# Kernel optimization log

Hardware: AMD Instinct MI355X
Metric: run time of the kernel (lower is better)

The kernel has to match this reference:

```python
import jax, jax.numpy as jnp
import numpy as np
import math

NH, NKV, D = 32, 8, 128  # heads, kv heads, head dim

def _alibi_slopes(n):
    cp2 = 2 ** math.floor(math.log2(n))
    base = 2.0 ** (-8.0 / cp2)
    slopes = base ** np.arange(1, cp2 + 1, dtype=np.float32)
    if cp2 != n:
        extra_base = 2.0 ** (-4.0 / cp2)
        extra = extra_base ** np.arange(1, 1 + 2 * (n - cp2), 2, dtype=np.float32)
        slopes = np.concatenate([slopes, extra])
    return slopes.astype(np.float32)

def setup_inputs() -> dict:
    key = jax.random.key(0)
    k1, k2, k3 = jax.random.split(key, 3)
    B, S, H = 4, 1024, 4096
    qkv_out = NH * D + 2 * NKV * D  # 6144
    return {
        "hidden_states": jax.random.normal(k1, (B, S, H), jnp.float32) * 0.02,
        "w_qkv": jax.random.normal(k2, (H, qkv_out), jnp.float32) * 0.02,
        "w_o": jax.random.normal(k3, (NH * D, H), jnp.float32) * 0.02,
    }

def reference(hidden_states, w_qkv, w_o):
    B, S, H = hidden_states.shape
    G = NH // NKV  # query groups per kv head
    scale = D ** -0.5

    qkv = hidden_states @ w_qkv  # [B,S,6144]
    q = qkv[..., : NH * D].reshape(B, S, NKV, G, D)
    k = qkv[..., NH * D : NH * D + NKV * D].reshape(B, S, NKV, D)
    v = qkv[..., NH * D + NKV * D :].reshape(B, S, NKV, D)

    scores = jnp.einsum("bqhgd,bkhd->bhgqk", q, k) * scale  # [B,NKV,G,S,S]

    slopes = jnp.asarray(_alibi_slopes(NH)).reshape(NKV, G)  # head order
    pos = jnp.arange(S)
    rel = pos[:, None] - pos[None, :]  # i - j
    sqrt_dist = jnp.sqrt(jnp.maximum(rel, 0).astype(jnp.float32))
    bias = -slopes[:, :, None, None] * sqrt_dist  # ALiBi-sqrt bias
    bias = jnp.where(rel[None, None] >= 0, bias, -jnp.inf)  # causal mask

    attn = jax.nn.softmax(scores + bias[None], axis=-1)
    out = jnp.einsum("bhgqk,bkhd->bqhgd", attn, v).reshape(B, S, NH * D)
    return out @ w_o
```

## Files before the change

kernel.cpp:

```cpp
#include <hip/hip_runtime.h>
#include <stdint.h>

typedef __attribute__((ext_vector_type(4))) float floatx4;
typedef __attribute__((ext_vector_type(8))) short short8;
typedef unsigned short ushort_t;

#define DEVI __device__ __forceinline__

constexpr int Bc   = 4;
constexpr int Sc   = 1024;
constexpr int Hc   = 4096;
constexpr int NHc  = 32;
constexpr int NKVc = 8;
constexpr int Dc   = 128;
constexpr int QKVO = 6144;
constexpr int Mc   = Bc * Sc;

DEVI ushort_t f2bf(float f) {
  union { float f; unsigned u; } x; x.f = f;
  unsigned u = x.u;
  u += 0x7fffu + ((u >> 16) & 1u);
  return (ushort_t)(u >> 16);
}

DEVI short8 cvt8(floatx4 a, floatx4 b) {
  short8 r;
  r[0] = (short)f2bf(a[0]); r[1] = (short)f2bf(a[1]);
  r[2] = (short)f2bf(a[2]); r[3] = (short)f2bf(a[3]);
  r[4] = (short)f2bf(b[0]); r[5] = (short)f2bf(b[1]);
  r[6] = (short)f2bf(b[2]); r[7] = (short)f2bf(b[3]);
  return r;
}

DEVI void load_lds16(const ushort_t* g, ushort_t* l) {
  __builtin_amdgcn_global_load_lds(
      (const __attribute__((address_space(1))) void*)g,
      (__attribute__((address_space(3))) void*)l, 16, 0, 0);
}

__global__ __launch_bounds__(256)
void cvt_bf16(const float* __restrict__ src, ushort_t* __restrict__ dst, int n8)
{
  const int i = blockIdx.x * 256 + threadIdx.x;
  if (i >= n8) return;
  const floatx4 f0 = *(const floatx4*)(src + (size_t)i * 8);
  const floatx4 f1 = *(const floatx4*)(src + (size_t)i * 8 + 4);
  *(short8*)(dst + (size_t)i * 8) = cvt8(f0, f1);
}

__global__ __launch_bounds__(256)
void transpose_cvt(const float* __restrict__ src, ushort_t* __restrict__ dst,
                   int R, int C)
{
  __shared__ float ts[64][67];
  const int cb = C >> 6;
  const int r0 = (blockIdx.x / cb) << 6;
  const int c0 = (blockIdx.x % cb) << 6;
  const int t  = threadIdx.x;

  const int lr = t >> 4, lc = (t & 15) << 2;
#pragma unroll
  for (int i = 0; i < 4; ++i) {
    const floatx4 v = *(const floatx4*)(src + (size_t)(r0 + lr + 16 * i) * C + c0 + lc);
#pragma unroll
    for (int j = 0; j < 4; ++j) ts[lr + 16 * i][lc + j] = v[j];
  }
  __syncthreads();

  const int c     = ((t >> 6) << 4) + ((t & 63) >> 2);
  const int chunk = t & 3;
  short8 t0, t1;
#pragma unroll
  for (int k = 0; k < 8; ++k) t0[k] = (short)f2bf(ts[chunk * 16 + k][c]);
#pragma unroll
  for (int k = 0; k < 8; ++k) t1[k] = (short)f2bf(ts[chunk * 16 + 8 + k][c]);
  ushort_t* dp = dst + (size_t)(c0 + c) * R + r0 + chunk * 16;
  *(short8*)dp       = t0;
  *(short8*)(dp + 8) = t1;
}

__global__ __launch_bounds__(256)
void v_transpose(const ushort_t* __restrict__ qkv, ushort_t* __restrict__ vt)
{
  __shared__ ushort_t ts[64][72];
  const int bid = blockIdx.x;
  const int db  = bid & 1;
  const int sb  = (bid >> 1) & 15;
  const int hkv = (bid >> 5) & 7;
  const int b   = bid >> 8;
  const int t   = threadIdx.x;

  const ushort_t* src = qkv + (size_t)(b * Sc + sb * 64) * QKVO
                        + (NHc * Dc + NKVc * Dc) + hkv * Dc + db * 64;
  const int lr = t >> 3, lc = (t & 7) * 8;
  *(short8*)&ts[lr][lc]      = *(const short8*)(src + (size_t)lr * QKVO + lc);
  *(short8*)&ts[lr + 32][lc] = *(const short8*)(src + (size_t)(lr + 32) * QKVO + lc);
  __syncthreads();

  ushort_t* dst = vt + ((size_t)(b * NKVc + hkv) * Dc + db * 64) * Sc + sb * 64;
  const int dr  = t >> 2;
  const int sc0 = (t & 3) * 16;
  short8 o0, o1;
#pragma unroll
  for (int k = 0; k < 8; ++k) o0[k] = (short)ts[sc0 + k][dr];
#pragma unroll
  for (int k = 0; k < 8; ++k) o1[k] = (short)ts[sc0 + 8 + k][dr];
  *(short8*)(dst + (size_t)dr * Sc + sc0)     = o0;
  *(short8*)(dst + (size_t)dr * Sc + sc0 + 8) = o1;
}

template<bool OBF16>
__global__ __launch_bounds__(256)
void gemm_nt(const ushort_t* __restrict__ A, const ushort_t* __restrict__ BT,
             void* __restrict__ Cp, int M, int N, int K)
{
  __shared__ __align__(16) ushort_t As[128 * 64];
  __shared__ __align__(16) ushort_t Bs[128 * 64];

  const int nb  = N >> 7;
  const int nwg = (M >> 7) * nb;
  int bid = blockIdx.x;
  bid = (bid & 7) * (nwg >> 3) + (bid >> 3);
  const int bm = bid / nb, bn = bid % nb;
  const int m0 = bm << 7, n0 = bn << 7;

  const int tid  = threadIdx.x;
  const int wid  = tid >> 6, lane = tid & 63;
  const int wr   = (wid >> 1) << 6, wc = (wid & 1) << 6;
  const int fr   = lane & 15;
  const int srow = lane >> 3;
  const int scol = ((lane & 7) << 4) ^ (srow << 4);
  const int rsw  = (fr & 7) << 4;
  const int kb16 = (lane >> 4) << 4;

  const ushort_t* ag = A  + (size_t)(m0 + wid * 32 + srow) * K + (scol >> 1);
  const ushort_t* bg = BT + (size_t)(n0 + wid * 32 + srow) * K + (scol >> 1);
  ushort_t* as_u = &As[wid * 4 * 512];
  ushort_t* bs_u = &Bs[wid * 4 * 512];

  const floatx4 fz = {0.f, 0.f, 0.f, 0.f};
  floatx4 acc[4][4];
#pragma unroll
  for (int i = 0; i < 4; ++i)
#pragma unroll
    for (int j = 0; j < 4; ++j) acc[i][j] = fz;

  const char* Ab = (const char*)As + (size_t)(wr + fr) * 128;
  const char* Bb = (const char*)Bs + (size_t)(wc + fr) * 128;

  for (int k0 = 0; k0 < K; k0 += 64) {
#pragma unroll
    for (int i = 0; i < 4; ++i)
      load_lds16(ag + (size_t)i * 8 * K + k0, as_u + i * 512);
#pragma unroll
    for (int i = 0; i < 4; ++i)
      load_lds16(bg + (size_t)i * 8 * K + k0, bs_u + i * 512);
    __syncthreads();

#pragma unroll
    for (int ks = 0; ks < 2; ++ks) {
      const int co = (ks * 64 + kb16) ^ rsw;
      short8 af[4], bf[4];
#pragma unroll
      for (int i = 0; i < 4; ++i) af[i] = *(const short8*)(Ab + i * 2048 + co);
#pragma unroll
      for (int j = 0; j < 4; ++j) bf[j] = *(const short8*)(Bb + j * 2048 + co);
#pragma unroll
      for (int i = 0; i < 4; ++i)
#pragma unroll
        for (int j = 0; j < 4; ++j)
          acc[i][j] = __builtin_amdgcn_mfma_f32_16x16x32_bf16(af[i], bf[j],
                                                              acc[i][j], 0, 0, 0);
    }
    __syncthreads();
  }

  const int r4 = (lane >> 4) << 2;
#pragma unroll
  for (int i = 0; i < 4; ++i) {
#pragma unroll
    for (int rr = 0; rr < 4; ++rr) {
      const size_t row = (size_t)(m0 + wr + i * 16 + r4 + rr);
#pragma unroll
      for (int j = 0; j < 4; ++j) {
        const size_t col = (size_t)(n0 + wc + j * 16 + fr);
        if constexpr (OBF16)
          ((ushort_t*)Cp)[row * N + col] = f2bf(acc[i][j][rr]);
        else
          ((float*)Cp)[row * N + col] = acc[i][j][rr];
      }
    }
  }
}

__global__ __launch_bounds__(256, 2)
void attn_fwd(const ushort_t* __restrict__ qkv,
              const ushort_t* __restrict__ vt,
              ushort_t* __restrict__ attn)
{
  __shared__ __align__(16) ushort_t Plds[4][32 * 40];

  const int bid = blockIdx.x;
  const int x   = bid & 7;
  const int p   = bid >> 3;
  const int j   = p & 15;
  const int g   = ((p >> 4) << 3) + x;
  const int b   = g >> 3;
  const int hkv = g & 7;

  const int tid  = threadIdx.x;
  const int wid  = tid >> 6, lane = tid & 63;
  const int h    = hkv * 4 + wid;
  const int fr   = lane & 15;
  const int kk8  = (lane >> 4) << 3;
  const int q4   = (lane >> 4) << 2;
  const float slope = exp2f(-0.25f * (float)(h + 1));
  const float scale = 0.08838834764831845f;

  const ushort_t* qp  = qkv + (size_t)b * Sc * QKVO + (size_t)h * Dc;
  const ushort_t* kp  = qkv + (size_t)b * Sc * QKVO + NHc * Dc + (size_t)hkv * Dc;
  const ushort_t* vtp = vt + (size_t)(b * NKVc + hkv) * Dc * Sc;
  ushort_t* myP = &Plds[wid][0];

  const floatx4 fz = {0.f, 0.f, 0.f, 0.f};

  auto process = [&](const int qb) {
    short8 qf[2][4];
#pragma unroll
    for (int t = 0; t < 2; ++t) {
      const int qrow = qb * 32 + t * 16 + fr;
#pragma unroll
      for (int s = 0; s < 4; ++s)
        qf[t][s] = *(const short8*)(qp + (size_t)qrow * QKVO + s * 32 + kk8);
    }

    floatx4 o[2][8];
#pragma unroll
    for (int t = 0; t < 2; ++t)
#pragma unroll
      for (int jj = 0; jj < 8; ++jj) o[t][jj] = fz;
    float mrow[2][4], lrow[2][4];
#pragma unroll
    for (int t = 0; t < 2; ++t)
#pragma unroll
      for (int rr = 0; rr < 4; ++rr) { mrow[t][rr] = -1e30f; lrow[t][rr] = 0.f; }

    for (int kb = 0; kb <= qb; ++kb) {
      floatx4 s_[2][2];
      s_[0][0] = fz; s_[0][1] = fz; s_[1][0] = fz; s_[1][1] = fz;
#pragma unroll
      for (int half = 0; half < 2; ++half) {
        const int kcol = kb * 32 + half * 16 + fr;
#pragma unroll
        for (int s = 0; s < 4; ++s) {
          const short8 kf = *(const short8*)(kp + (size_t)kcol * QKVO + s * 32 + kk8);
          s_[0][half] = __builtin_amdgcn_mfma_f32_16x16x32_bf16(qf[0][s], kf, s_[0][half], 0, 0, 0);
          s_[1][half] = __builtin_amdgcn_mfma_f32_16x16x32_bf16(qf[1][s], kf, s_[1][half], 0, 0, 0);
        }
      }

      short8 vf[8];
#pragma unroll
      for (int jj = 0; jj < 8; ++jj)
        vf[jj] = *(const short8*)(vtp + (size_t)(jj * 16 + fr) * Sc + kb * 32 + kk8);

#pragma unroll
      for (int t = 0; t < 2; ++t)
#pragma unroll
        for (int rr = 0; rr < 4; ++rr) {
          const int qg  = qb * 32 + t * 16 + q4 + rr;
          const int dk0 = qg - (kb * 32 + fr);
          const int dk1 = dk0 - 16;
          s_[t][0][rr] = (dk0 >= 0)
              ? s_[t][0][rr] * scale - slope * sqrtf((float)dk0) : -1e30f;
          s_[t][1][rr] = (dk1 >= 0)
              ? s_[t][1][rr] * scale - slope * sqrtf((float)dk1) : -1e30f;
        }

      float pmv[2][4];
#pragma unroll
      for (int t = 0; t < 2; ++t)
#pragma unroll
        for (int rr = 0; rr < 4; ++rr) {
          float pm = fmaxf(s_[t][0][rr], s_[t][1][rr]);
#pragma unroll
          for (int m = 1; m < 16; m <<= 1) pm = fmaxf(pm, __shfl_xor(pm, m));
          pmv[t][rr] = pm;
        }

      int need = 0;
#pragma unroll
      for (int t = 0; t < 2; ++t)
#pragma unroll
        for (int rr = 0; rr < 4; ++rr)
          need |= (pmv[t][rr] > mrow[t][rr] + 8.f) ? 1 : 0;
      if (__any(need)) {
#pragma unroll
        for (int t = 0; t < 2; ++t)
#pragma unroll
          for (int rr = 0; rr < 4; ++rr) {
            const float mnew = fmaxf(mrow[t][rr], pmv[t][rr]);
            const float corr = __expf(mrow[t][rr] - mnew);
            lrow[t][rr] *= corr;
            mrow[t][rr] = mnew;
#pragma unroll
            for (int jj = 0; jj < 8; ++jj) o[t][jj][rr] *= corr;
          }
      }

#pragma unroll
      for (int t = 0; t < 2; ++t)
#pragma unroll
        for (int rr = 0; rr < 4; ++rr) {
          const float p0 = __expf(s_[t][0][rr] - mrow[t][rr]);
          const float p1 = __expf(s_[t][1][rr] - mrow[t][rr]);
          lrow[t][rr] += p0 + p1;
          myP[(t * 16 + q4 + rr) * 40 + fr]      = f2bf(p0);
          myP[(t * 16 + q4 + rr) * 40 + 16 + fr] = f2bf(p1);
        }
      short8 pa[2];
      pa[0] = *(const short8*)&myP[fr * 40 + kk8];
      pa[1] = *(const short8*)&myP[(16 + fr) * 40 + kk8];

#pragma unroll
      for (int jj = 0; jj < 8; ++jj) {
        o[0][jj] = __builtin_amdgcn_mfma_f32_16x16x32_bf16(pa[0], vf[jj], o[0][jj], 0, 0, 0);
        o[1][jj] = __builtin_amdgcn_mfma_f32_16x16x32_bf16(pa[1], vf[jj], o[1][jj], 0, 0, 0);
      }
    }

#pragma unroll
    for (int t = 0; t < 2; ++t)
#pragma unroll
      for (int rr = 0; rr < 4; ++rr) {
        float rs = lrow[t][rr];
#pragma unroll
        for (int m = 1; m < 16; m <<= 1) rs += __shfl_xor(rs, m);
        const float inv = 1.f / rs;
        const size_t tok = (size_t)b * Sc + qb * 32 + t * 16 + q4 + rr;
#pragma unroll
        for (int jj = 0; jj < 8; ++jj)
          attn[tok * (size_t)(NHc * Dc) + h * Dc + jj * 16 + fr] = f2bf(o[t][jj][rr] * inv);
      }
  };

  process(31 - j);
  process(j);
}

extern "C" void kernel_launch(void* const* d_in, const int* in_sizes, int n_in,
                              void* d_out, int out_size, void* d_ws, size_t ws_size,
                              hipStream_t stream)
{
  const float* hidden = (const float*)d_in[0];
  const float* w_qkv  = (const float*)d_in[1];
  const float* w_o    = (const float*)d_in[2];
  float* out = (float*)d_out;

  ushort_t* wqT   = (ushort_t*)d_ws;
  ushort_t* hidb  = wqT + (size_t)QKVO * Hc;
  ushort_t* qkvb  = hidb + (size_t)Mc * Hc;
  ushort_t* attnb = hidb;
  ushort_t* woT   = wqT;
  ushort_t* vtb   = wqT + (size_t)Mc * Hc;

  cvt_bf16<<<dim3((Mc * Hc / 8) / 256), dim3(256), 0, stream>>>(
      hidden, hidb, Mc * Hc / 8);
  transpose_cvt<<<dim3((Hc / 64) * (QKVO / 64)), dim3(256), 0, stream>>>(
      w_qkv, wqT, Hc, QKVO);
  gemm_nt<true><<<dim3((Mc / 128) * (QKVO / 128)), dim3(256), 0, stream>>>(
      hidb, wqT, qkvb, Mc, QKVO, Hc);
  v_transpose<<<dim3(1024), dim3(256), 0, stream>>>(qkvb, vtb);
  attn_fwd<<<dim3(512), dim3(256), 0, stream>>>(qkvb, vtb, attnb);
  transpose_cvt<<<dim3((Hc / 64) * (Hc / 64)), dim3(256), 0, stream>>>(
      w_o, woT, Hc, Hc);
  gemm_nt<false><<<dim3((Mc / 128) * (Hc / 128)), dim3(256), 0, stream>>>(
      attnb, woT, out, Mc, Hc, Hc);
}
```

Before: 642.6 us.

## Replace GEMM with 256x256 double-buffered, 8-wave ping-pong pipelined kernel

Both projection GEMMs move from a 128x128 tile with 4 waves and a single LDS buffer to a 256x256 tile with 8 waves, double-buffered LDS, and a four-phase schedule. In that schedule, next-tile global-to-LDS loads are interleaved with MFMA blocks under explicit barriers, waitcnts and setprio. The aim is to hide global load latency behind compute and raise arithmetic intensity per LDS byte. In exchange it uses 128KB of LDS per block and many more accumulator registers, which can limit occupancy. The grid also shrinks to 384 and 256 blocks, which may fill the CUs unevenly.

Measured after the change: 576.8 us. 10.2% less time.

```diff
diff --git a/kernel.cpp b/kernel.cpp
--- a/kernel.cpp
+++ b/kernel.cpp
@@ -38,6 +38,10 @@
       (__attribute__((address_space(3))) void*)l, 16, 0, 0);
 }
 
+#define BARRIER()  asm volatile("s_barrier" ::: "memory")
+#define LGKM0()    asm volatile("s_waitcnt lgkmcnt(0)" ::: "memory")
+#define VMCNT(n)   asm volatile("s_waitcnt vmcnt(" #n ")" ::: "memory")
+
 __global__ __launch_bounds__(256)
 void cvt_bf16(const float* __restrict__ src, ushort_t* __restrict__ dst, int n8)
 {
@@ -110,84 +114,160 @@
 }
 
 template<bool OBF16>
-__global__ __launch_bounds__(256)
-void gemm_nt(const ushort_t* __restrict__ A, const ushort_t* __restrict__ BT,
-             void* __restrict__ Cp, int M, int N, int K)
-{
-  __shared__ __align__(16) ushort_t As[128 * 64];
-  __shared__ __align__(16) ushort_t Bs[128 * 64];
-
-  const int nb  = N >> 7;
-  const int nwg = (M >> 7) * nb;
+__global__ __launch_bounds__(512, 2)
+void gemm_nt8(const ushort_t* __restrict__ A, const ushort_t* __restrict__ BT,
+              void* __restrict__ Cp, int M, int N, int K)
+{
+  __shared__ __align__(16) ushort_t As[2][256 * 64];
+  __shared__ __align__(16) ushort_t Bs[2][256 * 64];
+
+  const int nb  = N >> 8;
+  const int nwg = (M >> 8) * nb;
   int bid = blockIdx.x;
   bid = (bid & 7) * (nwg >> 3) + (bid >> 3);
   const int bm = bid / nb, bn = bid % nb;
-  const int m0 = bm << 7, n0 = bn << 7;
+  const int m0 = bm << 8, n0 = bn << 8;
 
   const int tid  = threadIdx.x;
   const int wid  = tid >> 6, lane = tid & 63;
-  const int wr   = (wid >> 1) << 6, wc = (wid & 1) << 6;
+  const int wm   = wid >> 2, wn = wid & 3;
   const int fr   = lane & 15;
-  const int srow = lane >> 3;
-  const int scol = ((lane & 7) << 4) ^ (srow << 4);
+  const int g16  = (lane >> 4) << 4;
   const int rsw  = (fr & 7) << 4;
-  const int kb16 = (lane >> 4) << 4;
-
-  const ushort_t* ag = A  + (size_t)(m0 + wid * 32 + srow) * K + (scol >> 1);
-  const ushort_t* bg = BT + (size_t)(n0 + wid * 32 + srow) * K + (scol >> 1);
-  ushort_t* as_u = &As[wid * 4 * 512];
-  ushort_t* bs_u = &Bs[wid * 4 * 512];
+  const int l8   = lane >> 3;
+  const int scol = ((lane & 7) ^ l8) << 3;
+
+  const int arow0 = wm * 128 + wn * 32;
+  const int brow0 = (((wn >> 1) << 3) + ((wm * 2 + (wn & 1)) << 1)) * 16;
+
+  const ushort_t* agl = A  + (size_t)(m0 + arow0 + l8) * K + scol;
+  const ushort_t* bgl = BT + (size_t)(n0 + brow0 + l8) * K + scol;
+
+  const int rowA = (wm * 128 + fr) * 128;
+  const int rowB = (wn * 64 + fr) * 128;
+  const int cb0  = g16 ^ rsw;
+  const int cb1  = (64 + g16) ^ rsw;
 
   const floatx4 fz = {0.f, 0.f, 0.f, 0.f};
-  floatx4 acc[4][4];
-#pragma unroll
-  for (int i = 0; i < 4; ++i)
-#pragma unroll
-    for (int j = 0; j < 4; ++j) acc[i][j] = fz;
-
-  const char* Ab = (const char*)As + (size_t)(wr + fr) * 128;
-  const char* Bb = (const char*)Bs + (size_t)(wc + fr) * 128;
-
-  for (int k0 = 0; k0 < K; k0 += 64) {
+  floatx4 acc[8][4];
+#pragma unroll
+  for (int i = 0; i < 8; ++i)
+#pragma unroll
+    for (int f = 0; f < 4; ++f) acc[i][f] = fz;
+
+  load_lds16(agl,                  &As[0][(arow0 +  0) * 64]);
+  load_lds16(agl +  8 * (size_t)K, &As[0][(arow0 +  8) * 64]);
+  load_lds16(agl + 16 * (size_t)K, &As[0][(arow0 + 16) * 64]);
+  load_lds16(agl + 24 * (size_t)K, &As[0][(arow0 + 24) * 64]);
+  load_lds16(bgl,                  &Bs[0][(brow0 +  0) * 64]);
+  load_lds16(bgl +  8 * (size_t)K, &Bs[0][(brow0 +  8) * 64]);
+  load_lds16(bgl + 16 * (size_t)K, &Bs[0][(brow0 + 16) * 64]);
+  load_lds16(bgl + 24 * (size_t)K, &Bs[0][(brow0 + 24) * 64]);
+  VMCNT(0);
+  BARRIER();
+
+  const int NT = K >> 6;
+  for (int kt = 0; kt < NT; ++kt) {
+    const int u = kt & 1, v = u ^ 1;
+    const char* Au = (const char*)&As[u][0];
+    const char* Bu = (const char*)&Bs[u][0];
+    const bool st  = (kt + 1 < NT);
+    const size_t kn = (size_t)(kt + 1) << 6;
+
+#define LDA(i, ks) (*(const short8*)(Au + rowA + (i) * 2048 + ((ks) ? cb1 : cb0)))
+#define LDB(f, ks) (*(const short8*)(Bu + rowB + (f) * 2048 + ((ks) ? cb1 : cb0)))
+#define MFMA16(d, a0, a1, b0, b1)                                         \
+    d = __builtin_amdgcn_mfma_f32_16x16x32_bf16(a0, b0, d, 0, 0, 0);      \
+    d = __builtin_amdgcn_mfma_f32_16x16x32_bf16(a1, b1, d, 0, 0, 0);
+
+    short8 aR[4][2], bE[2][2], bO[2][2];
+
+#pragma unroll
+    for (int i = 0; i < 4; ++i) { aR[i][0] = LDA(i, 0); aR[i][1] = LDA(i, 1); }
+#pragma unroll
+    for (int f = 0; f < 2; ++f) { bE[f][0] = LDB(2 * f, 0); bE[f][1] = LDB(2 * f, 1); }
+    if (st) {
+      load_lds16(agl + kn,                 &As[v][(arow0 + 0) * 64]);
+      load_lds16(agl + 8 * (size_t)K + kn, &As[v][(arow0 + 8) * 64]);
+    }
+    BARRIER();
+    __builtin_amdgcn_s_setprio(1);
 #pragma unroll
     for (int i = 0; i < 4; ++i)
-      load_lds16(ag + (size_t)i * 8 * K + k0, as_u + i * 512);
+#pragma unroll
+      for (int f = 0; f < 2; ++f) { MFMA16(acc[i][2 * f], aR[i][0], aR[i][1], bE[f][0], bE[f][1]); }
+    __builtin_amdgcn_s_setprio(0);
+    LGKM0();
+    BARRIER();
+
+#pragma unroll
+    for (int i = 0; i < 4; ++i) { aR[i][0] = LDA(4 + i, 0); aR[i][1] = LDA(4 + i, 1); }
+    if (st) {
+      load_lds16(agl + 16 * (size_t)K + kn, &As[v][(arow0 + 16) * 64]);
+      load_lds16(agl + 24 * (size_t)K + kn, &As[v][(arow0 + 24) * 64]);
+    }
+    BARRIER();
+    __builtin_amdgcn_s_setprio(1);
 #pragma unroll
     for (int i = 0; i < 4; ++i)
-      load_lds16(bg + (size_t)i * 8 * K + k0, bs_u + i * 512);
-    __syncthreads();
-
-#pragma unroll
-    for (int ks = 0; ks < 2; ++ks) {
-      const int co = (ks * 64 + kb16) ^ rsw;
-      short8 af[4], bf[4];
-#pragma unroll
-      for (int i = 0; i < 4; ++i) af[i] = *(const short8*)(Ab + i * 2048 + co);
-#pragma unroll
-      for (int j = 0; j < 4; ++j) bf[j] = *(const short8*)(Bb + j * 2048 + co);
-#pragma unroll
-      for (int i = 0; i < 4; ++i)
-#pragma unroll
-        for (int j = 0; j < 4; ++j)
-          acc[i][j] = __builtin_amdgcn_mfma_f32_16x16x32_bf16(af[i], bf[j],
-                                                              acc[i][j], 0, 0, 0);
-    }
-    __syncthreads();
+#pragma unroll
+      for (int f = 0; f < 2; ++f) { MFMA16(acc[4 + i][2 * f], aR[i][0], aR[i][1], bE[f][0], bE[f][1]); }
+    __builtin_amdgcn_s_setprio(0);
+    LGKM0();
+    if (st) { VMCNT(4); } else { VMCNT(0); }
+    BARRIER();
+
+#pragma unroll
+    for (int f = 0; f < 2; ++f) { bO[f][0] = LDB(2 * f + 1, 0); bO[f][1] = LDB(2 * f + 1, 1); }
+    if (st) {
+      load_lds16(bgl + kn,                 &Bs[v][(brow0 + 0) * 64]);
+      load_lds16(bgl + 8 * (size_t)K + kn, &Bs[v][(brow0 + 8) * 64]);
+    }
+    BARRIER();
+    __builtin_amdgcn_s_setprio(1);
+#pragma unroll
+    for (int i = 0; i < 4; ++i)
+#pragma unroll
+      for (int f = 0; f < 2; ++f) { MFMA16(acc[4 + i][2 * f + 1], aR[i][0], aR[i][1], bO[f][0], bO[f][1]); }
+    __builtin_amdgcn_s_setprio(0);
+    LGKM0();
+    BARRIER();
+
+#pragma unroll
+    for (int i = 0; i < 4; ++i) { aR[i][0] = LDA(i, 0); aR[i][1] = LDA(i, 1); }
+    if (st) {
+      load_lds16(bgl + 16 * (size_t)K + kn, &Bs[v][(brow0 + 16) * 64]);
+      load_lds16(bgl + 24 * (size_t)K + kn, &Bs[v][(brow0 + 24) * 64]);
+    }
+    BARRIER();
+    __builtin_amdgcn_s_setprio(1);
+#pragma unroll
+    for (int i = 0; i < 4; ++i)
+#pragma unroll
+      for (int f = 0; f < 2; ++f) { MFMA16(acc[i][2 * f + 1], aR[i][0], aR[i][1], bO[f][0], bO[f][1]); }
+    __builtin_amdgcn_s_setprio(0);
+    LGKM0();
+    VMCNT(2);
+    BARRIER();
+
+#undef LDA
+#undef LDB
+#undef MFMA16
   }
 
   const int r4 = (lane >> 4) << 2;
 #pragma unroll
-  for (int i = 0; i < 4; ++i) {
+  for (int i = 0; i < 8; ++i) {
 #pragma unroll
     for (int rr = 0; rr < 4; ++rr) {
-      const size_t row = (size_t)(m0 + wr + i * 16 + r4 + rr);
-#pragma unroll
-      for (int j = 0; j < 4; ++j) {
-        const size_t col = (size_t)(n0 + wc + j * 16 + fr);
+      const size_t row = (size_t)(m0 + wm * 128 + i * 16 + r4 + rr);
+#pragma unroll
+      for (int f = 0; f < 4; ++f) {
+        const size_t col = (size_t)(n0 + wn * 64 + f * 16 + fr);
         if constexpr (OBF16)
-          ((ushort_t*)Cp)[row * N + col] = f2bf(acc[i][j][rr]);
+          ((ushort_t*)Cp)[row * N + col] = f2bf(acc[i][f][rr]);
         else
-          ((float*)Cp)[row * N + col] = acc[i][j][rr];
+          ((float*)Cp)[row * N + col] = acc[i][f][rr];
       }
     }
   }
@@ -368,12 +448,12 @@
       hidden, hidb, Mc * Hc / 8);
   transpose_cvt<<<dim3((Hc / 64) * (QKVO / 64)), dim3(256), 0, stream>>>(
       w_qkv, wqT, Hc, QKVO);
-  gemm_nt<true><<<dim3((Mc / 128) * (QKVO / 128)), dim3(256), 0, stream>>>(
+  gemm_nt8<true><<<dim3((Mc / 256) * (QKVO / 256)), dim3(512), 0, stream>>>(
       hidb, wqT, qkvb, Mc, QKVO, Hc);
   v_transpose<<<dim3(1024), dim3(256), 0, stream>>>(qkvb, vtb);
   attn_fwd<<<dim3(512), dim3(256), 0, stream>>>(qkvb, vtb, attnb);
   transpose_cvt<<<dim3((Hc / 64) * (Hc / 64)), dim3(256), 0, stream>>>(
       w_o, woT, Hc, Hc);
-  gemm_nt<false><<<dim3((Mc / 128) * (Hc / 128)), dim3(256), 0, stream>>>(
+  gemm_nt8<false><<<dim3((Mc / 256) * (Hc / 256)), dim3(512), 0, stream>>>(
       attnb, woT, out, Mc, Hc, Hc);
 }
```
